# Optimization experiments

Hardware: AMD Instinct MI355X
Metric: run time of the kernel (lower is better)

## Reference

```python
import jax, jax.numpy as jnp
from jax import lax
import numpy as np

B, H, W, C = 8, 192, 192, 64   # decoder feature map at crop_layer 0 (NHWC)
N = 1024                       # total detections across the batch (flattened ragged)
S = 32                         # crop_size
NCLS = 3                       # n_cls
CH = 64                        # conv_channels


def setup_inputs() -> dict:
    key = jax.random.key(0)
    ks = jax.random.split(key, 12)
    features = jax.random.normal(ks[0], (B, H, W, C), jnp.float32)
    # normalized [y1, x1, y2, x2] boxes, well-formed and inside the image
    cy = jax.random.uniform(ks[1], (N,), minval=0.2, maxval=0.8)
    cx = jax.random.uniform(ks[2], (N,), minval=0.2, maxval=0.8)
    sy = jax.random.uniform(ks[3], (N,), minval=0.05, maxval=0.3)
    sx = jax.random.uniform(ks[4], (N,), minval=0.05, maxval=0.3)
    boxes = jnp.stack([
        jnp.clip(cy - sy / 2, 0.0, 1.0),
        jnp.clip(cx - sx / 2, 0.0, 1.0),
        jnp.clip(cy + sy / 2, 0.0, 1.0),
        jnp.clip(cx + sx / 2, 0.0, 1.0),
    ], axis=-1).astype(jnp.float32)
    box_ids = jax.random.randint(ks[5], (N,), 0, B, dtype=jnp.int32)
    cls = jax.random.randint(ks[6], (N,), 0, NCLS, dtype=jnp.int32)
    scale = 0.05
    conv1_w = jax.random.normal(ks[7], (3, 3, C, CH), jnp.float32) * scale
    conv1_b = jnp.zeros((CH,), jnp.float32)
    conv2_w = jax.random.normal(ks[8], (3, 3, CH, CH), jnp.float32) * scale
    conv2_b = jnp.zeros((CH,), jnp.float32)
    out_w = jax.random.normal(ks[9], (3, 3, CH, NCLS), jnp.float32) * scale
    out_b = jnp.zeros((NCLS,), jnp.float32)
    return dict(features=features, boxes=boxes, box_ids=box_ids, cls=cls,
                conv1_w=conv1_w, conv1_b=conv1_b, conv2_w=conv2_w, conv2_b=conv2_b,
                out_w=out_w, out_b=out_b)


def _crop_and_resize(features, boxes, box_ids, size):
    """tf.image.crop_and_resize-style bilinear per-box crop. -> [N, size, size, C]"""
    Hh, Ww = features.shape[1], features.shape[2]
    y1, x1, y2, x2 = boxes[:, 0], boxes[:, 1], boxes[:, 2], boxes[:, 3]
    t = jnp.arange(size, dtype=features.dtype) / (size - 1)
    ys = (y1[:, None] + t[None, :] * (y2 - y1)[:, None]) * (Hh - 1)  # [N,S]
    xs = (x1[:, None] + t[None, :] * (x2 - x1)[:, None]) * (Ww - 1)  # [N,S]
    y0 = jnp.clip(jnp.floor(ys), 0, Hh - 1)
    x0 = jnp.clip(jnp.floor(xs), 0, Ww - 1)
    wy = (ys - y0)[:, :, None, None]   # [N,S,1,1]
    wx = (xs - x0)[:, None, :, None]   # [N,1,S,1]
    y0i = y0.astype(jnp.int32); x0i = x0.astype(jnp.int32)
    y1i = jnp.minimum(y0i + 1, Hh - 1); x1i = jnp.minimum(x0i + 1, Ww - 1)
    b = box_ids[:, None, None]
    def g(yi, xi):  # gather [N,S,S,C]
        return features[b, yi[:, :, None], xi[:, None, :]]
    v00, v01 = g(y0i, x0i), g(y0i, x1i)
    v10, v11 = g(y1i, x0i), g(y1i, x1i)
    top = v00 * (1 - wx) + v01 * wx
    bot = v10 * (1 - wx) + v11 * wx
    return top * (1 - wy) + bot * wy


def _conv(x, w, b, pad):
    return lax.conv_general_dilated(x, w, (1, 1), pad,
                                    dimension_numbers=('NHWC', 'HWIO', 'NHWC')) + b


def reference(features, boxes, box_ids, cls, conv1_w, conv1_b, conv2_w, conv2_b, out_w, out_b):
    x = _crop_and_resize(features, boxes, box_ids, S)            # [N,32,32,C]
    x = jax.nn.relu(_conv(x, conv1_w, conv1_b, 'SAME'))          # mask_conv1
    x = jax.nn.relu(_conv(x, conv2_w, conv2_b, 'SAME'))          # mask_conv1 (second)
    m = _conv(x, out_w, out_b, 'VALID')                          # [N,30,30,n_cls]
    # batched class-channel gather: tf.gather(masks, cls[:,None], axis=-1, batch_dims=1)
    masks = m[jnp.arange(m.shape[0]), :, :, cls][..., None]      # [N,30,30,1]
    return masks
```

## Files before the change

kernel.cpp:

```cpp
#include <hip/hip_runtime.h>

#define HH 192
#define WW 192
#define CC 64
#define NB 1024
#define SS 32

typedef __bf16 bf16x8 __attribute__((ext_vector_type(8)));
typedef float  f32x4  __attribute__((ext_vector_type(4)));

__device__ __forceinline__ unsigned short f2bf(float f) {
    unsigned int u = __builtin_bit_cast(unsigned int, f);
    u += 0x7FFFu + ((u >> 16) & 1u);
    return (unsigned short)(u >> 16);
}

__global__ __launch_bounds__(256) void wt_kernel(const float* __restrict__ w,
                                                 unsigned short* __restrict__ wt) {
    int idx = blockIdx.x * 256 + threadIdx.x;
    int j    = idx & 7;
    int lane = (idx >> 3) & 63;
    int nt   = (idx >> 9) & 3;
    int kc   = (idx >> 11) & 1;
    int tap  = idx >> 12;
    int c = kc * 32 + ((lane >> 4) << 3) + j;
    int o = (nt << 4) + (lane & 15);
    wt[idx] = f2bf(w[(tap * 64 + c) * 64 + o]);
}

__global__ __launch_bounds__(256) void wto_kernel(const float* __restrict__ ow,
                                                  unsigned short* __restrict__ wto) {
    int idx = blockIdx.x * 256 + threadIdx.x;
    int j    = idx & 7;
    int lane = (idx >> 3) & 63;
    int kc   = (idx >> 9) & 1;
    int tap  = idx >> 10;
    int c = kc * 32 + ((lane >> 4) << 3) + j;
    int o = lane & 15;
    wto[idx] = (o < 3) ? f2bf(ow[(tap * 64 + c) * 3 + o]) : (unsigned short)0;
}

__global__ __launch_bounds__(256, 3) void crop_conv1_kernel(
        const float* __restrict__ feat, const float* __restrict__ boxes,
        const int* __restrict__ box_ids, const unsigned short* __restrict__ wt,
        const float* __restrict__ bias, unsigned short* __restrict__ out, int n0) {
    __shared__ unsigned short s_in[10 * 32 * 72];

    int nl = blockIdx.y;
    int gn = n0 + nl;
    int y0 = blockIdx.x << 3;
    int t = threadIdx.x;
    int wave = t >> 6, lane = t & 63;
    int quad = lane >> 4, mcol = lane & 15;

    {
        int px = t >> 3, cg = t & 7, c0 = cg << 3;
        float by1 = boxes[gn * 4 + 0];
        float bx1 = boxes[gn * 4 + 1];
        float by2 = boxes[gn * 4 + 2];
        float bx2 = boxes[gn * 4 + 3];
        float tx = (float)px / 31.0f;
        float xs = (bx1 + tx * (bx2 - bx1)) * 191.0f;
        float x0f = fminf(fmaxf(floorf(xs), 0.0f), 191.0f);
        float wx = xs - x0f;
        int x0i = (int)x0f, x1i = min(x0i + 1, 191);
        const float* fb = feat + (size_t)box_ids[gn] * (HH * WW * CC);
        unsigned short* dst = s_in + px * 72 + c0;
#pragma unroll 2
        for (int r = 0; r < 10; r++) {
            int gy = y0 + r - 1;
            uint4 v = {0, 0, 0, 0};
            if (gy >= 0 && gy < 32) {
                float ty = (float)gy / 31.0f;
                float ys = (by1 + ty * (by2 - by1)) * 191.0f;
                float y0f = fminf(fmaxf(floorf(ys), 0.0f), 191.0f);
                float wy = ys - y0f;
                int y0i = (int)y0f, y1i = min(y0i + 1, 191);
                const float* p00 = fb + ((size_t)y0i * WW + x0i) * CC + c0;
                const float* p01 = fb + ((size_t)y0i * WW + x1i) * CC + c0;
                const float* p10 = fb + ((size_t)y1i * WW + x0i) * CC + c0;
                const float* p11 = fb + ((size_t)y1i * WW + x1i) * CC + c0;
                unsigned int rr[4];
#pragma unroll
                for (int h = 0; h < 2; h++) {
                    float4 v00 = *(const float4*)(p00 + 4 * h);
                    float4 v01 = *(const float4*)(p01 + 4 * h);
                    float4 v10 = *(const float4*)(p10 + 4 * h);
                    float4 v11 = *(const float4*)(p11 + 4 * h);
                    const float* a00 = (const float*)&v00;
                    const float* a01 = (const float*)&v01;
                    const float* a10 = (const float*)&v10;
                    const float* a11 = (const float*)&v11;
#pragma unroll
                    for (int i = 0; i < 4; i++) {
                        float top = a00[i] + wx * (a01[i] - a00[i]);
                        float bot = a10[i] + wx * (a11[i] - a10[i]);
                        float val = top + wy * (bot - top);
                        unsigned short b = f2bf(val);
                        int e = 4 * h + i;
                        if (e & 1) rr[e >> 1] |= ((unsigned int)b << 16);
                        else       rr[e >> 1]  = (unsigned int)b;
                    }
                }
                v = *(uint4*)rr;
            }
            *(uint4*)(dst + r * 32 * 72) = v;
        }
    }
    __syncthreads();

    f32x4 acc[4][4];
#pragma unroll
    for (int nt = 0; nt < 4; nt++) {
        float bv = bias[(nt << 4) + mcol];
#pragma unroll
        for (int mi = 0; mi < 4; mi++) acc[mi][nt] = (f32x4){bv, bv, bv, bv};
    }

    int r0 = wave << 1;
#pragma unroll
    for (int dy = 0; dy < 3; dy++) {
#pragma unroll
        for (int dx = 0; dx < 3; dx++) {
            int tap = dy * 3 + dx;
#pragma unroll
            for (int kc = 0; kc < 2; kc++) {
                uint4 bfr[4];
#pragma unroll
                for (int nt = 0; nt < 4; nt++)
                    bfr[nt] = *(const uint4*)(wt + ((((tap * 2 + kc) * 4 + nt) * 64 + lane) << 3));
                uint4 afr[4];
#pragma unroll
                for (int mi = 0; mi < 4; mi++) {
                    int xs = ((mi & 1) << 4) + mcol + dx - 1;
                    uint4 a = {0, 0, 0, 0};
                    if (xs >= 0 && xs < 32)
                        a = *(const uint4*)(s_in + ((r0 + (mi >> 1) + dy) * 32 + xs) * 72 +
                                            (kc << 5) + (quad << 3));
                    afr[mi] = a;
                }
#pragma unroll
                for (int mi = 0; mi < 4; mi++)
#pragma unroll
                    for (int nt = 0; nt < 4; nt++)
                        acc[mi][nt] = __builtin_amdgcn_mfma_f32_16x16x32_bf16(
                            __builtin_bit_cast(bf16x8, afr[mi]),
                            __builtin_bit_cast(bf16x8, bfr[nt]), acc[mi][nt], 0, 0, 0);
            }
        }
    }

#pragma unroll
    for (int mi = 0; mi < 4; mi++) {
        int yy = y0 + r0 + (mi >> 1);
        int xb = ((mi & 1) << 4) + (quad << 2);
#pragma unroll
        for (int reg = 0; reg < 4; reg++) {
            unsigned short* op = out + (((size_t)nl * 32 + yy) * 32 + (xb + reg)) * 64 + mcol;
#pragma unroll
            for (int nt = 0; nt < 4; nt++) {
                float v = fmaxf(acc[mi][nt][reg], 0.0f);
                op[nt << 4] = f2bf(v);
            }
        }
    }
}

__global__ __launch_bounds__(256, 3) void conv3x3_kernel(const unsigned short* __restrict__ in,
                                                         const unsigned short* __restrict__ wt,
                                                         const float* __restrict__ bias,
                                                         unsigned short* __restrict__ out) {
    __shared__ unsigned short s_in[10 * 32 * 72];

    int nl = blockIdx.y;
    int y0 = blockIdx.x << 3;
    int t = threadIdx.x;
    int wave = t >> 6, lane = t & 63;
    int quad = lane >> 4, mcol = lane & 15;

    {
        int px = t >> 3, cc = (t & 7) << 3;
        const unsigned short* src = in + (((size_t)nl * 32) * 32 + px) * 64 + cc;
#pragma unroll
        for (int r = 0; r < 10; r++) {
            int gy = y0 + r - 1;
            uint4 v = {0, 0, 0, 0};
            if (gy >= 0 && gy < 32) v = *(const uint4*)(src + (size_t)gy * 32 * 64);
            *(uint4*)(s_in + (r * 32 + px) * 72 + cc) = v;
        }
    }
    __syncthreads();

    f32x4 acc[4][4];
#pragma unroll
    for (int nt = 0; nt < 4; nt++) {
        float bv = bias[(nt << 4) + mcol];
#pragma unroll
        for (int mi = 0; mi < 4; mi++) acc[mi][nt] = (f32x4){bv, bv, bv, bv};
    }

    int r0 = wave << 1;
#pragma unroll
    for (int dy = 0; dy < 3; dy++) {
#pragma unroll
        for (int dx = 0; dx < 3; dx++) {
            int tap = dy * 3 + dx;
#pragma unroll
            for (int kc = 0; kc < 2; kc++) {
                uint4 bfr[4];
#pragma unroll
                for (int nt = 0; nt < 4; nt++)
                    bfr[nt] = *(const uint4*)(wt + ((((tap * 2 + kc) * 4 + nt) * 64 + lane) << 3));
                uint4 afr[4];
#pragma unroll
                for (int mi = 0; mi < 4; mi++) {
                    int xs = ((mi & 1) << 4) + mcol + dx - 1;
                    uint4 a = {0, 0, 0, 0};
                    if (xs >= 0 && xs < 32)
                        a = *(const uint4*)(s_in + ((r0 + (mi >> 1) + dy) * 32 + xs) * 72 +
                                            (kc << 5) + (quad << 3));
                    afr[mi] = a;
                }
#pragma unroll
                for (int mi = 0; mi < 4; mi++)
#pragma unroll
                    for (int nt = 0; nt < 4; nt++)
                        acc[mi][nt] = __builtin_amdgcn_mfma_f32_16x16x32_bf16(
                            __builtin_bit_cast(bf16x8, afr[mi]),
                            __builtin_bit_cast(bf16x8, bfr[nt]), acc[mi][nt], 0, 0, 0);
            }
        }
    }

#pragma unroll
    for (int mi = 0; mi < 4; mi++) {
        int yy = y0 + r0 + (mi >> 1);
        int xb = ((mi & 1) << 4) + (quad << 2);
#pragma unroll
        for (int reg = 0; reg < 4; reg++) {
            unsigned short* op = out + (((size_t)nl * 32 + yy) * 32 + (xb + reg)) * 64 + mcol;
#pragma unroll
            for (int nt = 0; nt < 4; nt++) {
                float v = fmaxf(acc[mi][nt][reg], 0.0f);
                op[nt << 4] = f2bf(v);
            }
        }
    }
}

__global__ __launch_bounds__(256, 3) void outconv_mfma_kernel(const unsigned short* __restrict__ in,
                                                              const unsigned short* __restrict__ wto,
                                                              const float* __restrict__ ob,
                                                              const int* __restrict__ cls,
                                                              float* __restrict__ out, int n0) {
    __shared__ unsigned short s_act[10 * 32 * 72];

    int nl = blockIdx.y;
    int y0 = blockIdx.x << 3;
    int t = threadIdx.x;
    int wave = t >> 6, lane = t & 63;
    int quad = lane >> 4, mcol = lane & 15;

    {
        int px = t >> 3, cc = (t & 7) << 3;
        const unsigned short* src = in + (((size_t)nl * 32) * 32 + px) * 64 + cc;
#pragma unroll
        for (int r = 0; r < 10; r++) {
            int gy = y0 + r;
            uint4 v = {0, 0, 0, 0};
            if (gy < 32) v = *(const uint4*)(src + (size_t)gy * 32 * 64);
            *(uint4*)(s_act + (r * 32 + px) * 72 + cc) = v;
        }
    }
    __syncthreads();

    f32x4 acc[4];
#pragma unroll
    for (int mi = 0; mi < 4; mi++) acc[mi] = (f32x4){0.f, 0.f, 0.f, 0.f};

    int r0 = wave << 1;
#pragma unroll
    for (int dy = 0; dy < 3; dy++) {
#pragma unroll
        for (int dx = 0; dx < 3; dx++) {
            int tap = dy * 3 + dx;
#pragma unroll
            for (int kc = 0; kc < 2; kc++) {
                uint4 bfr = *(const uint4*)(wto + (((tap * 2 + kc) * 64 + lane) << 3));
#pragma unroll
                for (int mi = 0; mi < 4; mi++) {
                    int xs = ((mi & 1) << 4) + mcol + dx;
                    if (xs > 31) xs = 31;
                    uint4 a = *(const uint4*)(s_act + ((r0 + (mi >> 1) + dy) * 32 + xs) * 72 +
                                              (kc << 5) + (quad << 3));
                    acc[mi] = __builtin_amdgcn_mfma_f32_16x16x32_bf16(
                        __builtin_bit_cast(bf16x8, a),
                        __builtin_bit_cast(bf16x8, bfr), acc[mi], 0, 0, 0);
                }
            }
        }
    }

    int gn = n0 + nl;
    int oc = cls[gn];
    if (mcol == oc) {
        float bias = ob[oc];
#pragma unroll
        for (int mi = 0; mi < 4; mi++) {
            int yy = y0 + r0 + (mi >> 1);
            int xb = ((mi & 1) << 4) + (quad << 2);
            if (yy < 30) {
#pragma unroll
                for (int reg = 0; reg < 4; reg++) {
                    int x = xb + reg;
                    if (x < 30)
                        out[(size_t)gn * 900 + yy * 30 + x] = acc[mi][reg] + bias;
                }
            }
        }
    }
}

extern "C" void kernel_launch(void* const* d_in, const int* in_sizes, int n_in,
                              void* d_out, int out_size, void* d_ws, size_t ws_size,
                              hipStream_t stream) {
    const float* feat    = (const float*)d_in[0];
    const float* boxes   = (const float*)d_in[1];
    const int*   box_ids = (const int*)d_in[2];
    const int*   cls     = (const int*)d_in[3];
    const float* c1w     = (const float*)d_in[4];
    const float* c1b     = (const float*)d_in[5];
    const float* c2w     = (const float*)d_in[6];
    const float* c2b     = (const float*)d_in[7];
    const float* ow      = (const float*)d_in[8];
    const float* ob      = (const float*)d_in[9];

    unsigned short* wt1  = (unsigned short*)d_ws;
    unsigned short* wt2  = wt1 + 36864;
    unsigned short* wto  = wt2 + 36864;
    unsigned short* bufs = wto + 9216;

    size_t wt_bytes = (size_t)(36864 * 2 + 9216) * 2;
    size_t avail = (ws_size > wt_bytes) ? (ws_size - wt_bytes) / 2 : 0;
    size_t per_box = (size_t)32 * 32 * 64 * 2;
    int nc = (int)(avail / per_box);
    if (nc >= NB) nc = NB;
    else {
        int p = 1;
        while (p * 2 <= nc) p *= 2;
        nc = (p < 1) ? 1 : p;
    }

    wt_kernel<<<144, 256, 0, stream>>>(c1w, wt1);
    wt_kernel<<<144, 256, 0, stream>>>(c2w, wt2);
    wto_kernel<<<36, 256, 0, stream>>>(ow, wto);

    unsigned short* bufA = bufs;
    unsigned short* bufB = bufs + (size_t)nc * 65536;

    for (int nn0 = 0; nn0 < NB; nn0 += nc) {
        int cur = (NB - nn0 < nc) ? (NB - nn0) : nc;
        crop_conv1_kernel<<<dim3(4, cur), 256, 0, stream>>>(feat, boxes, box_ids,
                                                            wt1, c1b, bufA, nn0);
        conv3x3_kernel<<<dim3(4, cur), 256, 0, stream>>>(bufA, wt2, c2b, bufB);
        outconv_mfma_kernel<<<dim3(4, cur), 256, 0, stream>>>(bufB, wto, ob, cls,
                                                              (float*)d_out, nn0);
    }
}
```

Baseline: 379.4 us.

## Fuse conv2 and output conv into one kernel with halo recompute in LDS

Merges the second 3x3 conv and the class output conv into a single kernel. Each block loads a 12-row input halo, computes 10 rows of conv2 (5 M-tiles per wave), writes the ReLU'd bf16 result back into shared memory, then runs the output conv from LDS. This removes the global write and re-read of the conv2 activation buffer and one kernel launch. In exchange it recomputes overlapping halo rows, uses more LDS and more accumulator registers, and drops occupancy from 3 to 2 blocks per CU. Freeing the second buffer also lets larger chunks of boxes fit in the workspace.

```diff
diff --git a/kernel.cpp b/kernel.cpp
--- a/kernel.cpp
+++ b/kernel.cpp
@@ -166,11 +166,12 @@
     }
 }
 
-__global__ __launch_bounds__(256, 3) void conv3x3_kernel(const unsigned short* __restrict__ in,
-                                                         const unsigned short* __restrict__ wt,
-                                                         const float* __restrict__ bias,
-                                                         unsigned short* __restrict__ out) {
-    __shared__ unsigned short s_in[10 * 32 * 72];
+__global__ __launch_bounds__(256, 2) void conv2_out_kernel(
+        const unsigned short* __restrict__ in, const unsigned short* __restrict__ wt,
+        const float* __restrict__ bias, const unsigned short* __restrict__ wto,
+        const float* __restrict__ ob, const int* __restrict__ cls,
+        float* __restrict__ out, int n0) {
+    __shared__ unsigned short s_in[12 * 32 * 72];
 
     int nl = blockIdx.y;
     int y0 = blockIdx.x << 3;
@@ -182,24 +183,27 @@
         int px = t >> 3, cc = (t & 7) << 3;
         const unsigned short* src = in + (((size_t)nl * 32) * 32 + px) * 64 + cc;
 #pragma unroll
-        for (int r = 0; r < 10; r++) {
+        for (int r = 0; r < 12; r++) {
             int gy = y0 + r - 1;
             uint4 v = {0, 0, 0, 0};
-            if (gy >= 0 && gy < 32) v = *(const uint4*)(src + (size_t)gy * 32 * 64);
+            if (gy >= 0 && gy < 32) v = *(const uint4*)(src + (size_t)gy * 2048);
             *(uint4*)(s_in + (r * 32 + px) * 72 + cc) = v;
         }
     }
     __syncthreads();
 
-    f32x4 acc[4][4];
-#pragma unroll
-    for (int nt = 0; nt < 4; nt++) {
-        float bv = bias[(nt << 4) + mcol];
-#pragma unroll
-        for (int mi = 0; mi < 4; mi++) acc[mi][nt] = (f32x4){bv, bv, bv, bv};
-    }
-
-    int r0 = wave << 1;
+    float bv[4];
+#pragma unroll
+    for (int nt = 0; nt < 4; nt++) bv[nt] = bias[(nt << 4) + mcol];
+
+    f32x4 acc[5][4];
+#pragma unroll
+    for (int i = 0; i < 5; i++)
+#pragma unroll
+        for (int nt = 0; nt < 4; nt++)
+            acc[i][nt] = (f32x4){bv[nt], bv[nt], bv[nt], bv[nt]};
+
+    int mt0 = wave * 5;
 #pragma unroll
     for (int dy = 0; dy < 3; dy++) {
 #pragma unroll
@@ -211,72 +215,47 @@
 #pragma unroll
                 for (int nt = 0; nt < 4; nt++)
                     bfr[nt] = *(const uint4*)(wt + ((((tap * 2 + kc) * 4 + nt) * 64 + lane) << 3));
-                uint4 afr[4];
-#pragma unroll
-                for (int mi = 0; mi < 4; mi++) {
-                    int xs = ((mi & 1) << 4) + mcol + dx - 1;
+#pragma unroll
+                for (int i = 0; i < 5; i++) {
+                    int mt = mt0 + i;
+                    int lr = mt >> 1, h = mt & 1;
+                    int xs = (h << 4) + mcol + dx - 1;
                     uint4 a = {0, 0, 0, 0};
                     if (xs >= 0 && xs < 32)
-                        a = *(const uint4*)(s_in + ((r0 + (mi >> 1) + dy) * 32 + xs) * 72 +
+                        a = *(const uint4*)(s_in + ((lr + dy) * 32 + xs) * 72 +
                                             (kc << 5) + (quad << 3));
-                    afr[mi] = a;
-                }
-#pragma unroll
-                for (int mi = 0; mi < 4; mi++)
 #pragma unroll
                     for (int nt = 0; nt < 4; nt++)
-                        acc[mi][nt] = __builtin_amdgcn_mfma_f32_16x16x32_bf16(
-                            __builtin_bit_cast(bf16x8, afr[mi]),
-                            __builtin_bit_cast(bf16x8, bfr[nt]), acc[mi][nt], 0, 0, 0);
-            }
-        }
-    }
-
-#pragma unroll
-    for (int mi = 0; mi < 4; mi++) {
-        int yy = y0 + r0 + (mi >> 1);
-        int xb = ((mi & 1) << 4) + (quad << 2);
+                        acc[i][nt] = __builtin_amdgcn_mfma_f32_16x16x32_bf16(
+                            __builtin_bit_cast(bf16x8, a),
+                            __builtin_bit_cast(bf16x8, bfr[nt]), acc[i][nt], 0, 0, 0);
+                }
+            }
+        }
+    }
+    __syncthreads();
+
+#pragma unroll
+    for (int i = 0; i < 5; i++) {
+        int mt = mt0 + i;
+        int lr = mt >> 1, h = mt & 1;
+        int xb = (h << 4) + (quad << 2);
 #pragma unroll
         for (int reg = 0; reg < 4; reg++) {
-            unsigned short* op = out + (((size_t)nl * 32 + yy) * 32 + (xb + reg)) * 64 + mcol;
+            int px = xb + reg;
 #pragma unroll
             for (int nt = 0; nt < 4; nt++) {
-                float v = fmaxf(acc[mi][nt][reg], 0.0f);
-                op[nt << 4] = f2bf(v);
-            }
-        }
-    }
-}
-
-__global__ __launch_bounds__(256, 3) void outconv_mfma_kernel(const unsigned short* __restrict__ in,
-                                                              const unsigned short* __restrict__ wto,
-                                                              const float* __restrict__ ob,
-                                                              const int* __restrict__ cls,
-                                                              float* __restrict__ out, int n0) {
-    __shared__ unsigned short s_act[10 * 32 * 72];
-
-    int nl = blockIdx.y;
-    int y0 = blockIdx.x << 3;
-    int t = threadIdx.x;
-    int wave = t >> 6, lane = t & 63;
-    int quad = lane >> 4, mcol = lane & 15;
-
-    {
-        int px = t >> 3, cc = (t & 7) << 3;
-        const unsigned short* src = in + (((size_t)nl * 32) * 32 + px) * 64 + cc;
-#pragma unroll
-        for (int r = 0; r < 10; r++) {
-            int gy = y0 + r;
-            uint4 v = {0, 0, 0, 0};
-            if (gy < 32) v = *(const uint4*)(src + (size_t)gy * 32 * 64);
-            *(uint4*)(s_act + (r * 32 + px) * 72 + cc) = v;
+                int oc = (nt << 4) + mcol;
+                float v = fmaxf(acc[i][nt][reg], 0.0f);
+                s_in[(lr * 32 + px) * 72 + oc] = f2bf(v);
+            }
         }
     }
     __syncthreads();
 
-    f32x4 acc[4];
-#pragma unroll
-    for (int mi = 0; mi < 4; mi++) acc[mi] = (f32x4){0.f, 0.f, 0.f, 0.f};
+    f32x4 acc2[4];
+#pragma unroll
+    for (int mi = 0; mi < 4; mi++) acc2[mi] = (f32x4){0.f, 0.f, 0.f, 0.f};
 
     int r0 = wave << 1;
 #pragma unroll
@@ -291,11 +270,11 @@
                 for (int mi = 0; mi < 4; mi++) {
                     int xs = ((mi & 1) << 4) + mcol + dx;
                     if (xs > 31) xs = 31;
-                    uint4 a = *(const uint4*)(s_act + ((r0 + (mi >> 1) + dy) * 32 + xs) * 72 +
+                    uint4 a = *(const uint4*)(s_in + ((r0 + (mi >> 1) + dy) * 32 + xs) * 72 +
                                               (kc << 5) + (quad << 3));
-                    acc[mi] = __builtin_amdgcn_mfma_f32_16x16x32_bf16(
+                    acc2[mi] = __builtin_amdgcn_mfma_f32_16x16x32_bf16(
                         __builtin_bit_cast(bf16x8, a),
-                        __builtin_bit_cast(bf16x8, bfr), acc[mi], 0, 0, 0);
+                        __builtin_bit_cast(bf16x8, bfr), acc2[mi], 0, 0, 0);
                 }
             }
         }
@@ -304,7 +283,7 @@
     int gn = n0 + nl;
     int oc = cls[gn];
     if (mcol == oc) {
-        float bias = ob[oc];
+        float obv = ob[oc];
 #pragma unroll
         for (int mi = 0; mi < 4; mi++) {
             int yy = y0 + r0 + (mi >> 1);
@@ -314,7 +293,7 @@
                 for (int reg = 0; reg < 4; reg++) {
                     int x = xb + reg;
                     if (x < 30)
-                        out[(size_t)gn * 900 + yy * 30 + x] = acc[mi][reg] + bias;
+                        out[(size_t)gn * 900 + yy * 30 + x] = acc2[mi][reg] + obv;
                 }
             }
         }
@@ -338,10 +317,10 @@
     unsigned short* wt1  = (unsigned short*)d_ws;
     unsigned short* wt2  = wt1 + 36864;
     unsigned short* wto  = wt2 + 36864;
-    unsigned short* bufs = wto + 9216;
+    unsigned short* bufA = wto + 9216;
 
     size_t wt_bytes = (size_t)(36864 * 2 + 9216) * 2;
-    size_t avail = (ws_size > wt_bytes) ? (ws_size - wt_bytes) / 2 : 0;
+    size_t avail = (ws_size > wt_bytes) ? (ws_size - wt_bytes) : 0;
     size_t per_box = (size_t)32 * 32 * 64 * 2;
     int nc = (int)(avail / per_box);
     if (nc >= NB) nc = NB;
@@ -355,15 +334,11 @@
     wt_kernel<<<144, 256, 0, stream>>>(c2w, wt2);
     wto_kernel<<<36, 256, 0, stream>>>(ow, wto);
 
-    unsigned short* bufA = bufs;
-    unsigned short* bufB = bufs + (size_t)nc * 65536;
-
     for (int nn0 = 0; nn0 < NB; nn0 += nc) {
         int cur = (NB - nn0 < nc) ? (NB - nn0) : nc;
         crop_conv1_kernel<<<dim3(4, cur), 256, 0, stream>>>(feat, boxes, box_ids,
                                                             wt1, c1b, bufA, nn0);
-        conv3x3_kernel<<<dim3(4, cur), 256, 0, stream>>>(bufA, wt2, c2b, bufB);
-        outconv_mfma_kernel<<<dim3(4, cur), 256, 0, stream>>>(bufB, wto, ob, cls,
-                                                              (float*)d_out, nn0);
-    }
-}
+        conv2_out_kernel<<<dim3(4, cur), 256, 0, stream>>>(bufA, wt2, c2b, wto, ob,
+                                                           cls, (float*)d_out, nn0);
+    }
+}
```

Result: faster. 356.8 us (-6.0%).
